# Kernel tuning notes

Measured on AMD Instinct MI355X. Metric: run time of the kernel, lower is better.

Reference implementation:

```python
import jax, jax.numpy as jnp
import numpy as np

EPS = 1e-05

def setup_inputs() -> dict:
    key = jax.random.key(0)
    k1, = jax.random.split(key, 1)
    x = jax.random.normal(k1, (4, 4096, 2048), dtype=jnp.float32)
    g = jnp.ones((2048,), dtype=jnp.float32)
    return {"x": x, "g": g}

def reference(x, g):
    # RMSNorm: x / sqrt(mean(x^2, axis=-1) + eps) * g, computed in fp32
    dtype = x.dtype
    xf = x.astype(jnp.float32)
    ms = jnp.mean(xf * xf, axis=-1, keepdims=True)  # [B,S,1]
    out = xf * jax.lax.rsqrt(ms + EPS) * g
    return out.astype(dtype)
```

## Files before the change

### kernel.cpp

```cpp
#include <hip/hip_runtime.h>

#define ROW_LEN 2048
#define BLOCK   256
#define EPS     1e-5f

__global__ __launch_bounds__(BLOCK) void RMSNorm_56607668961691_kernel(
    const float* __restrict__ x,
    const float* __restrict__ g,
    float* __restrict__ out)
{
    const int row = blockIdx.x;
    const int tid = threadIdx.x;

    const float4* __restrict__ xr   = reinterpret_cast<const float4*>(x + (size_t)row * ROW_LEN);
    float4* __restrict__       outr = reinterpret_cast<float4*>(out + (size_t)row * ROW_LEN);
    const float4* __restrict__ gv   = reinterpret_cast<const float4*>(g);

    float4 a = xr[tid];
    float4 b = xr[tid + BLOCK];

    float ss = a.x * a.x + a.y * a.y + a.z * a.z + a.w * a.w
             + b.x * b.x + b.y * b.y + b.z * b.z + b.w * b.w;

    #pragma unroll
    for (int off = 32; off > 0; off >>= 1)
        ss += __shfl_down(ss, off, 64);

    __shared__ float wave_sums[BLOCK / 64];
    const int wave = tid >> 6;
    const int lane = tid & 63;
    if (lane == 0) wave_sums[wave] = ss;
    __syncthreads();

    const float total = wave_sums[0] + wave_sums[1] + wave_sums[2] + wave_sums[3];
    const float scale = rsqrtf(total * (1.0f / (float)ROW_LEN) + EPS);

    const float4 ga = gv[tid];
    const float4 gb = gv[tid + BLOCK];

    float4 oa, ob;
    oa.x = a.x * scale * ga.x;
    oa.y = a.y * scale * ga.y;
    oa.z = a.z * scale * ga.z;
    oa.w = a.w * scale * ga.w;
    ob.x = b.x * scale * gb.x;
    ob.y = b.y * scale * gb.y;
    ob.z = b.z * scale * gb.z;
    ob.w = b.w * scale * gb.w;

    outr[tid]         = oa;
    outr[tid + BLOCK] = ob;
}

extern "C" void kernel_launch(void* const* d_in, const int* in_sizes, int n_in,
                              void* d_out, int out_size, void* d_ws, size_t ws_size,
                              hipStream_t stream) {
    const float* x = (const float*)d_in[0];
    const float* g = (const float*)d_in[1];
    float* out = (float*)d_out;

    const int rows = in_sizes[0] / ROW_LEN;
    RMSNorm_56607668961691_kernel<<<rows, BLOCK, 0, stream>>>(x, g, out);
}
```

Baseline: 229.3 us.

## Map one wavefront per row to drop shared-memory reduction and block barrier

```diff
diff --git a/kernel.cpp b/kernel.cpp
--- a/kernel.cpp
+++ b/kernel.cpp
@@ -2,6 +2,7 @@
 
 #define ROW_LEN 2048
 #define BLOCK   256
+#define ROWS_PER_BLOCK 4
 #define EPS     1e-5f
 
 __global__ __launch_bounds__(BLOCK) void RMSNorm_56607668961691_kernel(
@@ -9,47 +10,44 @@
     const float* __restrict__ g,
     float* __restrict__ out)
 {
-    const int row = blockIdx.x;
-    const int tid = threadIdx.x;
+    const int wave = threadIdx.x >> 6;
+    const int lane = threadIdx.x & 63;
+    const size_t row = (size_t)blockIdx.x * ROWS_PER_BLOCK + wave;
 
-    const float4* __restrict__ xr   = reinterpret_cast<const float4*>(x + (size_t)row * ROW_LEN);
-    float4* __restrict__       outr = reinterpret_cast<float4*>(out + (size_t)row * ROW_LEN);
-    const float4* __restrict__ gv   = reinterpret_cast<const float4*>(g);
+    const float4* __restrict__ xr   = reinterpret_cast<const float4*>(x + row * ROW_LEN) + lane;
+    float4* __restrict__       outr = reinterpret_cast<float4*>(out + row * ROW_LEN) + lane;
+    const float4* __restrict__ gv   = reinterpret_cast<const float4*>(g) + lane;
 
-    float4 a = xr[tid];
-    float4 b = xr[tid + BLOCK];
+    float4 v[8];
+    #pragma unroll
+    for (int j = 0; j < 8; ++j) v[j] = xr[j * 64];
 
-    float ss = a.x * a.x + a.y * a.y + a.z * a.z + a.w * a.w
-             + b.x * b.x + b.y * b.y + b.z * b.z + b.w * b.w;
+    float s0 = 0.f, s1 = 0.f, s2 = 0.f, s3 = 0.f;
+    #pragma unroll
+    for (int j = 0; j < 8; ++j) {
+        s0 += v[j].x * v[j].x;
+        s1 += v[j].y * v[j].y;
+        s2 += v[j].z * v[j].z;
+        s3 += v[j].w * v[j].w;
+    }
+    float ss = (s0 + s1) + (s2 + s3);
 
     #pragma unroll
     for (int off = 32; off > 0; off >>= 1)
-        ss += __shfl_down(ss, off, 64);
+        ss += __shfl_xor(ss, off, 64);
 
-    __shared__ float wave_sums[BLOCK / 64];
-    const int wave = tid >> 6;
-    const int lane = tid & 63;
-    if (lane == 0) wave_sums[wave] = ss;
-    __syncthreads();
+    const float scale = rsqrtf(ss * (1.0f / (float)ROW_LEN) + EPS);
 
-    const float total = wave_sums[0] + wave_sums[1] + wave_sums[2] + wave_sums[3];
-    const float scale = rsqrtf(total * (1.0f / (float)ROW_LEN) + EPS);
-
-    const float4 ga = gv[tid];
-    const float4 gb = gv[tid + BLOCK];
-
-    float4 oa, ob;
-    oa.x = a.x * scale * ga.x;
-    oa.y = a.y * scale * ga.y;
-    oa.z = a.z * scale * ga.z;
-    oa.w = a.w * scale * ga.w;
-    ob.x = b.x * scale * gb.x;
-    ob.y = b.y * scale * gb.y;
-    ob.z = b.z * scale * gb.z;
-    ob.w = b.w * scale * gb.w;
-
-    outr[tid]         = oa;
-    outr[tid + BLOCK] = ob;
+    #pragma unroll
+    for (int j = 0; j < 8; ++j) {
+        const float4 gj = gv[j * 64];
+        float4 o;
+        o.x = v[j].x * scale * gj.x;
+        o.y = v[j].y * scale * gj.y;
+        o.z = v[j].z * scale * gj.z;
+        o.w = v[j].w * scale * gj.w;
+        outr[j * 64] = o;
+    }
 }
 
 extern "C" void kernel_launch(void* const* d_in, const int* in_sizes, int n_in,
@@ -60,5 +58,6 @@
     float* out = (float*)d_out;
 
     const int rows = in_sizes[0] / ROW_LEN;
-    RMSNorm_56607668961691_kernel<<<rows, BLOCK, 0, stream>>>(x, g, out);
+    const int grid = rows / ROWS_PER_BLOCK;
+    RMSNorm_56607668961691_kernel<<<grid, BLOCK, 0, stream>>>(x, g, out);
 }
```

Result: no change. 229.3 us (-0.0%).
